# Performance work log

Hardware: AMD Instinct MI355X
Metric: run time of the kernel (lower is better)

The kernel has to match this reference:

```python
import jax, jax.numpy as jnp
import numpy as np

E = 4096      # hidden_size
H = 32        # num_attention_heads
D = E // H    # head_dim = 128
PAST = 8191   # past kv length


def setup_inputs() -> dict:
    key = jax.random.key(0)
    ks = jax.random.split(key, 10)
    s = 0.02
    return {
        "hidden_states": jax.random.normal(ks[0], (1, 1, E), jnp.float32),
        "past_key": jax.random.normal(ks[1], (1, D, PAST), jnp.float32),
        "past_value": jax.random.normal(ks[2], (1, PAST, D), jnp.float32),
        "attention_mask": jnp.zeros((1, 1, 1, PAST + 1), jnp.float32),
        "q_w": jax.random.normal(ks[3], (E, E), jnp.float32) * s,
        "q_b": jnp.zeros((E,), jnp.float32),
        "kv_w": jax.random.normal(ks[4], (E, 2 * D), jnp.float32) * s,
        "kv_b": jnp.zeros((2 * D,), jnp.float32),
        "proj_w": jax.random.normal(ks[5], (E, E), jnp.float32) * s,
        "proj_b": jnp.zeros((E,), jnp.float32),
    }


def reference(hidden_states, past_key, past_value, attention_mask,
              q_w, q_b, kv_w, kv_b, proj_w, proj_b):
    B, S = hidden_states.shape[:2]  # B=1, S=1 (decode)
    # Conv1D projections: x @ W + b
    query = hidden_states @ q_w + q_b            # [B, S, E]
    kv = hidden_states @ kv_w + kv_b             # [B, S, 2D]
    key_new, value_new = kv[..., :D], kv[..., D:]  # [B, S, D] each

    q = query.reshape(B, S, H, D).transpose(0, 2, 1, 3)  # [B, H, S, D]
    key_perm = key_new.transpose(0, 2, 1)                 # [B, D, S]
    full_key = jnp.concatenate([past_key, key_perm], axis=-1)     # [B, D, K]
    full_value = jnp.concatenate([past_value, value_new], axis=-2)  # [B, K, D]
    K = full_key.shape[-1]

    # QK^T with shared single KV head, scaled by sqrt(head_dim)
    scores = jnp.einsum('bhqd,bdk->bhqk', q, full_key)  # [B, H, S, K]
    scores = scores / jnp.asarray(D ** 0.5, scores.dtype)

    # causal mask over rows [K-S, K)
    causal = (jnp.arange(K)[None, :] <= (jnp.arange(S) + (K - S))[:, None])  # [S, K]
    mask_value = jnp.asarray(jnp.finfo(scores.dtype).min, scores.dtype)
    scores = jnp.where(causal[None, None], scores, mask_value)
    scores = scores + attention_mask

    attn_weights = jax.nn.softmax(scores, axis=-1)                # [B, H, S, K]
    attn_out = jnp.einsum('bhqk,bkd->bhqd', attn_weights, full_value)  # [B, H, S, D]
    attn_out = attn_out.transpose(0, 2, 1, 3).reshape(B, S, E)    # merge heads
    attn_out = attn_out @ proj_w + proj_b                          # [B, S, E]
    return attn_out, key_perm, value_new
```

## Files before the change

kernel.cpp:

```cpp
#include <hip/hip_runtime.h>
#include <math.h>

#define E_DIM 4096
#define H_NUM 32
#define D_DIM 128
#define PAST_K 8191
#define K_TOT 8192

typedef float f32x4 __attribute__((ext_vector_type(4)));

#define WS_QUERY 0
#define WS_KV    4096
#define WS_PQ    4608
#define WS_PA    (WS_PQ + 256*4352)
#define WS_PL    (WS_PA + 128*4096)
#define WS_PP    (WS_PL + 4096)

__global__ void __launch_bounds__(576, 2)
k_qkv(const float* __restrict__ hs,
      const float* __restrict__ q_w,
      const float* __restrict__ kv_w,
      float* __restrict__ ws) {
    const int t = threadIdx.x;
    const int e0 = blockIdx.y * 16;
    if (t < 512) {
        const int o = blockIdx.x * 2048 + t * 4;
        float ax = 0.f, ay = 0.f, az = 0.f, aw = 0.f;
#pragma unroll
        for (int i = 0; i < 16; ++i) {
            const int e = e0 + i;
            const float x = hs[e];
            const float4 w = *reinterpret_cast<const float4*>(q_w + (size_t)e * E_DIM + o);
            ax += x * w.x; ay += x * w.y; az += x * w.z; aw += x * w.w;
        }
        *reinterpret_cast<float4*>(ws + WS_PQ + (size_t)blockIdx.y * 4352 + o) =
            make_float4(ax, ay, az, aw);
    } else if (blockIdx.x == 0) {
        const int o = (t - 512) * 4;
        float ax = 0.f, ay = 0.f, az = 0.f, aw = 0.f;
#pragma unroll
        for (int i = 0; i < 16; ++i) {
            const int e = e0 + i;
            const float x = hs[e];
            const float4 w = *reinterpret_cast<const float4*>(kv_w + (size_t)e * 256 + o);
            ax += x * w.x; ay += x * w.y; az += x * w.z; aw += x * w.w;
        }
        *reinterpret_cast<float4*>(ws + WS_PQ + (size_t)blockIdx.y * 4352 + 4096 + o) =
            make_float4(ax, ay, az, aw);
    }
}

__global__ void __launch_bounds__(256, 4)
k_qkv_reduce(const float* __restrict__ q_b, const float* __restrict__ kv_b,
             float* __restrict__ ws, float* __restrict__ out) {
    __shared__ f32x4 rr[32][8];
    const int t = threadIdx.x;
    const int ol = t & 7;
    const int sg = t >> 3;
    const int o = blockIdx.x * 32 + ol * 4;
    f32x4 acc = {0.f, 0.f, 0.f, 0.f};
#pragma unroll
    for (int s = sg * 8; s < sg * 8 + 8; ++s)
        acc += *reinterpret_cast<const f32x4*>(ws + WS_PQ + (size_t)s * 4352 + o);
    rr[sg][ol] = acc;
    __syncthreads();
    if (t < 8) {
        f32x4 v = {0.f, 0.f, 0.f, 0.f};
#pragma unroll
        for (int g = 0; g < 32; ++g) v += rr[g][t];
        const int oo = blockIdx.x * 32 + t * 4;
        if (oo < 4096) {
#pragma unroll
            for (int j = 0; j < 4; ++j) ws[WS_QUERY + oo + j] = v[j] + q_b[oo + j];
        } else {
            const int i = oo - 4096;
#pragma unroll
            for (int j = 0; j < 4; ++j) {
                const float r = v[j] + kv_b[i + j];
                ws[WS_KV + i + j] = r;
                out[oo + j] = r;
            }
        }
    }
}

__global__ void __launch_bounds__(512, 2)
k_attn(const float* __restrict__ past_key,
       const float* __restrict__ past_value,
       const float* __restrict__ mask,
       float* __restrict__ ws) {
    __shared__ float sq[8 * 128];
    __shared__ float sp[8 * 64];
    __shared__ float red[4096];
    const int t = threadIdx.x;
    const int hy = blockIdx.y;
    const int kx = blockIdx.x;
    const int h0 = hy * 8;
    const int k0 = kx * 64;
    const float* __restrict__ kvn = ws + WS_KV;

    sq[t]       = ws[WS_QUERY + h0 * D_DIM + t];
    sq[t + 512] = ws[WS_QUERY + h0 * D_DIM + t + 512];
    __syncthreads();

    const int kl = t & 63;
    const int team = t >> 6;
    const int d0 = team * 16;
    const int k = k0 + kl;
    const bool tailA = (k == PAST_K);
    const float* kp = tailA ? (kvn + d0) : (past_key + (size_t)d0 * PAST_K + k);
    const size_t kstr = tailA ? 1 : PAST_K;

    float acc[8];
#pragma unroll
    for (int h = 0; h < 8; ++h) acc[h] = 0.f;

#pragma unroll
    for (int i = 0; i < 16; i += 4) {
        const float v0 = kp[0];
        const float v1 = kp[kstr];
        const float v2 = kp[2 * kstr];
        const float v3 = kp[3 * kstr];
        kp += 4 * kstr;
#pragma unroll
        for (int h = 0; h < 8; ++h) {
            const float4 q = *reinterpret_cast<const float4*>(&sq[h * 128 + d0 + i]);
            acc[h] += q.x * v0 + q.y * v1 + q.z * v2 + q.w * v3;
        }
    }
#pragma unroll
    for (int h = 0; h < 8; ++h)
        red[(team * 8 + h) * 64 + kl] = acc[h];
    __syncthreads();

    {
        const float scale = 0.08838834764831845f;
        const float mk = mask[k];
        float s = 0.f;
#pragma unroll
        for (int tp = 0; tp < 8; ++tp) s += red[(tp * 8 + team) * 64 + kl];
        const float e = __expf(s * scale + mk);
        sp[team * 64 + kl] = e;
        float l = e;
#pragma unroll
        for (int off = 32; off > 0; off >>= 1) l += __shfl_xor(l, off);
        if (kl == 0)
            ws[WS_PL + ((size_t)(kx * 4 + hy)) * 8 + team] = l;
    }
    __syncthreads();

    const int d = t & 127;
    const int kg = t >> 7;
    const int kb = k0 + kg * 16;
    const float* __restrict__ vp = past_value + (size_t)kb * D_DIM + d;
    const float* __restrict__ vlast =
        (kb + 15 == PAST_K) ? (kvn + D_DIM + d) : (vp + 15 * (size_t)D_DIM);

    float b[8];
#pragma unroll
    for (int h = 0; h < 8; ++h) b[h] = 0.f;

#pragma unroll
    for (int kk = 0; kk < 15; ++kk) {
        const float v = vp[(size_t)kk * D_DIM];
#pragma unroll
        for (int h = 0; h < 8; ++h) b[h] += sp[h * 64 + kg * 16 + kk] * v;
    }
    {
        const float v = *vlast;
#pragma unroll
        for (int h = 0; h < 8; ++h) b[h] += sp[h * 64 + kg * 16 + 15] * v;
    }
#pragma unroll
    for (int h = 0; h < 8; ++h)
        red[(kg * 8 + h) * 128 + d] = b[h];
    __syncthreads();

#pragma unroll
    for (int j = 0; j < 2; ++j) {
        const int hh = kg * 2 + j;
        const float s = red[(0 * 8 + hh) * 128 + d] + red[(1 * 8 + hh) * 128 + d] +
                        red[(2 * 8 + hh) * 128 + d] + red[(3 * 8 + hh) * 128 + d];
        ws[WS_PA + (size_t)kx * 4096 + (h0 + hh) * D_DIM + d] = s;
    }
}

__global__ void __launch_bounds__(512, 2)
k_proj(const float* __restrict__ proj_w,
       float* __restrict__ ws) {
    __shared__ float sred[32 * 16];
    __shared__ float lpart[2];
    __shared__ float sa[16];
    const int t = threadIdx.x;
    const int by = blockIdx.y;
    const int e0 = by * 16;
    const int h  = by >> 3;

    {
        const int el = t & 15;
        const int kg = t >> 4;
        float ps = 0.f;
#pragma unroll
        for (int j = 0; j < 4; ++j)
            ps += ws[WS_PA + (size_t)(kg * 4 + j) * 4096 + e0 + el];
        sred[kg * 16 + el] = ps;
    }
    if (t < 128) {
        float lv = ws[WS_PL + (size_t)t * 32 + (h >> 3) * 8 + (h & 7)];
#pragma unroll
        for (int off = 32; off > 0; off >>= 1) lv += __shfl_xor(lv, off);
        if ((t & 63) == 0) lpart[t >> 6] = lv;
    }
    __syncthreads();
    if (t < 16) {
        float asum = 0.f;
#pragma unroll
        for (int g = 0; g < 32; ++g) asum += sred[g * 16 + t];
        sa[t] = asum / (lpart[0] + lpart[1]);
    }
    __syncthreads();

    const int o = blockIdx.x * 2048 + t * 4;
    float ax = 0.f, ay = 0.f, az = 0.f, aw = 0.f;
#pragma unroll
    for (int i = 0; i < 16; ++i) {
        const float x = sa[i];
        const float4 w = *reinterpret_cast<const float4*>(proj_w + (size_t)(e0 + i) * E_DIM + o);
        ax += x * w.x; ay += x * w.y; az += x * w.z; aw += x * w.w;
    }
    *reinterpret_cast<float4*>(ws + WS_PP + (size_t)by * 4096 + o) =
        make_float4(ax, ay, az, aw);
}

__global__ void __launch_bounds__(256, 4)
k_proj_reduce(const float* __restrict__ proj_b,
              float* __restrict__ ws, float* __restrict__ out) {
    __shared__ f32x4 rr[32][8];
    const int t = threadIdx.x;
    const int ol = t & 7;
    const int sg = t >> 3;
    const int o = blockIdx.x * 32 + ol * 4;
    f32x4 acc = {0.f, 0.f, 0.f, 0.f};
#pragma unroll
    for (int s = sg * 8; s < sg * 8 + 8; ++s)
        acc += *reinterpret_cast<const f32x4*>(ws + WS_PP + (size_t)s * 4096 + o);
    rr[sg][ol] = acc;
    __syncthreads();
    if (t < 8) {
        f32x4 v = {0.f, 0.f, 0.f, 0.f};
#pragma unroll
        for (int g = 0; g < 32; ++g) v += rr[g][t];
        const int oo = blockIdx.x * 32 + t * 4;
        const f32x4 bb = *reinterpret_cast<const f32x4*>(proj_b + oo);
        *reinterpret_cast<f32x4*>(out + oo) = v + bb;
    }
}

extern "C" void kernel_launch(void* const* d_in, const int* in_sizes, int n_in,
                              void* d_out, int out_size, void* d_ws, size_t ws_size,
                              hipStream_t stream) {
    const float* hs      = (const float*)d_in[0];
    const float* past_k  = (const float*)d_in[1];
    const float* past_v  = (const float*)d_in[2];
    const float* mask    = (const float*)d_in[3];
    const float* q_w     = (const float*)d_in[4];
    const float* q_b     = (const float*)d_in[5];
    const float* kv_w    = (const float*)d_in[6];
    const float* kv_b    = (const float*)d_in[7];
    const float* proj_w  = (const float*)d_in[8];
    const float* proj_b  = (const float*)d_in[9];
    float* out = (float*)d_out;
    float* ws  = (float*)d_ws;

    k_qkv        <<<dim3(2, 256), dim3(576), 0, stream>>>(hs, q_w, kv_w, ws);
    k_qkv_reduce <<<dim3(136),    dim3(256), 0, stream>>>(q_b, kv_b, ws, out);
    k_attn       <<<dim3(128, 4), dim3(512), 0, stream>>>(past_k, past_v, mask, ws);
    k_proj       <<<dim3(2, 256), dim3(512), 0, stream>>>(proj_w, ws);
    k_proj_reduce<<<dim3(128),    dim3(256), 0, stream>>>(proj_b, ws, out);
}
```

Before: 187.3 us.

## Fuse split-K GEMV and reduction kernels via inter-block flag synchronization

Merges the QKV GEMV with its reduction kernel, and the output projection GEMV with its reduction kernel, into single launches. Producer blocks publish partial sums with agent-scope atomic stores and set per-block flags; reducer blocks in the same grid spin on those flags. The flags are reset inside the attention kernel for the next call. Each producer block now handles 32 input rows instead of 16. This cuts launches from five to three and removes the tail gaps between them, at the cost of spin-waiting and relying on all blocks being co-resident to avoid deadlock.

```diff
diff --git a/kernel.cpp b/kernel.cpp
--- a/kernel.cpp
+++ b/kernel.cpp
@@ -12,73 +12,142 @@
 #define WS_QUERY 0
 #define WS_KV    4096
 #define WS_PQ    4608
-#define WS_PA    (WS_PQ + 256*4352)
+#define WS_PKV   (WS_PQ + 128*4096)
+#define WS_PA    (WS_PKV + 16*256)
 #define WS_PL    (WS_PA + 128*4096)
 #define WS_PP    (WS_PL + 4096)
-
-__global__ void __launch_bounds__(576, 2)
-k_qkv(const float* __restrict__ hs,
-      const float* __restrict__ q_w,
-      const float* __restrict__ kv_w,
-      float* __restrict__ ws) {
+#define WS_FLAGS (WS_PP + 128*4096)
+
+#define MAGIC  0x3A91C27D
+#define NFLAG1 272
+#define NFLAG3 256
+
+__device__ inline void st_agent_f2(float* p, float a, float b) {
+    union { float f[2]; unsigned long long u; } v;
+    v.f[0] = a; v.f[1] = b;
+    __hip_atomic_store(reinterpret_cast<unsigned long long*>(p), v.u,
+                       __ATOMIC_RELAXED, __HIP_MEMORY_SCOPE_AGENT);
+}
+
+__device__ inline void set_flag(int* f) {
+    asm volatile("" ::: "memory");
+    __hip_atomic_store(f, MAGIC, __ATOMIC_RELAXED, __HIP_MEMORY_SCOPE_AGENT);
+}
+
+__device__ inline void spin_flag(const int* f) {
+    while (__hip_atomic_load(f, __ATOMIC_RELAXED, __HIP_MEMORY_SCOPE_AGENT) != MAGIC)
+        __builtin_amdgcn_s_sleep(8);
+}
+
+__global__ void __launch_bounds__(512, 2)
+k_qkv_f(const float* __restrict__ hs,
+        const float* __restrict__ q_w,
+        const float* __restrict__ kv_w,
+        const float* __restrict__ q_b,
+        const float* __restrict__ kv_b,
+        float* __restrict__ ws, float* __restrict__ out) {
+    __shared__ f32x4 sm[576];
+    int* flags = reinterpret_cast<int*>(ws + WS_FLAGS);
+    const int id = blockIdx.x;
     const int t = threadIdx.x;
-    const int e0 = blockIdx.y * 16;
-    if (t < 512) {
-        const int o = blockIdx.x * 2048 + t * 4;
+
+    if (id < 256) {
+        const int strip = id >> 7;
+        const int by = id & 127;
+        const int e0 = by * 32;
+        const int o = strip * 2048 + t * 4;
         float ax = 0.f, ay = 0.f, az = 0.f, aw = 0.f;
 #pragma unroll
-        for (int i = 0; i < 16; ++i) {
-            const int e = e0 + i;
-            const float x = hs[e];
-            const float4 w = *reinterpret_cast<const float4*>(q_w + (size_t)e * E_DIM + o);
+        for (int i = 0; i < 32; ++i) {
+            const float x = hs[e0 + i];
+            const float4 w = *reinterpret_cast<const float4*>(q_w + (size_t)(e0 + i) * E_DIM + o);
             ax += x * w.x; ay += x * w.y; az += x * w.z; aw += x * w.w;
         }
-        *reinterpret_cast<float4*>(ws + WS_PQ + (size_t)blockIdx.y * 4352 + o) =
-            make_float4(ax, ay, az, aw);
-    } else if (blockIdx.x == 0) {
-        const int o = (t - 512) * 4;
+        float* p = ws + WS_PQ + (size_t)by * 4096 + o;
+        st_agent_f2(p, ax, ay);
+        st_agent_f2(p + 2, az, aw);
+        __syncthreads();
+        if (t == 0) set_flag(&flags[id]);
+    } else if (id < 272) {
+        const int k = id - 256;
+        const int ol = t & 63;
+        const int rg = t >> 6;
+        const int o = ol * 4;
         float ax = 0.f, ay = 0.f, az = 0.f, aw = 0.f;
 #pragma unroll
-        for (int i = 0; i < 16; ++i) {
-            const int e = e0 + i;
-            const float x = hs[e];
-            const float4 w = *reinterpret_cast<const float4*>(kv_w + (size_t)e * 256 + o);
+        for (int i = 0; i < 32; ++i) {
+            const int r = k * 256 + rg * 32 + i;
+            const float x = hs[r];
+            const float4 w = *reinterpret_cast<const float4*>(kv_w + (size_t)r * 256 + o);
             ax += x * w.x; ay += x * w.y; az += x * w.z; aw += x * w.w;
         }
-        *reinterpret_cast<float4*>(ws + WS_PQ + (size_t)blockIdx.y * 4352 + 4096 + o) =
-            make_float4(ax, ay, az, aw);
-    }
-}
-
-__global__ void __launch_bounds__(256, 4)
-k_qkv_reduce(const float* __restrict__ q_b, const float* __restrict__ kv_b,
-             float* __restrict__ ws, float* __restrict__ out) {
-    __shared__ f32x4 rr[32][8];
-    const int t = threadIdx.x;
-    const int ol = t & 7;
-    const int sg = t >> 3;
-    const int o = blockIdx.x * 32 + ol * 4;
-    f32x4 acc = {0.f, 0.f, 0.f, 0.f};
-#pragma unroll
-    for (int s = sg * 8; s < sg * 8 + 8; ++s)
-        acc += *reinterpret_cast<const f32x4*>(ws + WS_PQ + (size_t)s * 4352 + o);
-    rr[sg][ol] = acc;
-    __syncthreads();
-    if (t < 8) {
-        f32x4 v = {0.f, 0.f, 0.f, 0.f};
-#pragma unroll
-        for (int g = 0; g < 32; ++g) v += rr[g][t];
-        const int oo = blockIdx.x * 32 + t * 4;
-        if (oo < 4096) {
-#pragma unroll
-            for (int j = 0; j < 4; ++j) ws[WS_QUERY + oo + j] = v[j] + q_b[oo + j];
+        sm[rg * 64 + ol] = (f32x4){ax, ay, az, aw};
+        __syncthreads();
+        if (t < 64) {
+            f32x4 v = {0.f, 0.f, 0.f, 0.f};
+#pragma unroll
+            for (int g = 0; g < 8; ++g) v += sm[g * 64 + t];
+            float* p = ws + WS_PKV + k * 256 + t * 4;
+            st_agent_f2(p, v.x, v.y);
+            st_agent_f2(p + 2, v.z, v.w);
+        }
+        __syncthreads();
+        if (t == 0) set_flag(&flags[256 + k]);
+    } else {
+        const int c = id - 272;
+        if (c < 128) {
+            const int o0 = c * 32;
+            const int s = c >> 6;
+            if (t < 128) spin_flag(&flags[s * 128 + t]);
+            __syncthreads();
+            if (t == 0) (void)__hip_atomic_load(&flags[s * 128], __ATOMIC_ACQUIRE,
+                                                __HIP_MEMORY_SCOPE_AGENT);
+            __syncthreads();
+            const int ol = t & 7, sg = t >> 3;
+            const int o = o0 + ol * 4;
+            f32x4 acc = *reinterpret_cast<const f32x4*>(ws + WS_PQ + (size_t)(2 * sg) * 4096 + o)
+                      + *reinterpret_cast<const f32x4*>(ws + WS_PQ + (size_t)(2 * sg + 1) * 4096 + o);
+            sm[sg * 8 + ol] = acc;
+            __syncthreads();
+            if (t < 64) {
+                const int sup = t >> 3, l = t & 7;
+                f32x4 v = {0.f, 0.f, 0.f, 0.f};
+#pragma unroll
+                for (int j = 0; j < 8; ++j) v += sm[(sup * 8 + j) * 8 + l];
+                sm[512 + sup * 8 + l] = v;
+            }
+            __syncthreads();
+            if (t < 8) {
+                f32x4 v = {0.f, 0.f, 0.f, 0.f};
+#pragma unroll
+                for (int s2 = 0; s2 < 8; ++s2) v += sm[512 + s2 * 8 + t];
+                const int oo = o0 + t * 4;
+#pragma unroll
+                for (int j = 0; j < 4; ++j) ws[WS_QUERY + oo + j] = v[j] + q_b[oo + j];
+            }
         } else {
-            const int i = oo - 4096;
-#pragma unroll
-            for (int j = 0; j < 4; ++j) {
-                const float r = v[j] + kv_b[i + j];
-                ws[WS_KV + i + j] = r;
-                out[oo + j] = r;
+            const int o0k = (c - 128) * 32;
+            if (t < 16) spin_flag(&flags[256 + t]);
+            __syncthreads();
+            if (t == 0) (void)__hip_atomic_load(&flags[256], __ATOMIC_ACQUIRE,
+                                                __HIP_MEMORY_SCOPE_AGENT);
+            __syncthreads();
+            if (t < 128) {
+                const int ol = t & 7, sg = t >> 3;
+                sm[sg * 8 + ol] = *reinterpret_cast<const f32x4*>(ws + WS_PKV + sg * 256 + o0k + ol * 4);
+            }
+            __syncthreads();
+            if (t < 8) {
+                f32x4 v = {0.f, 0.f, 0.f, 0.f};
+#pragma unroll
+                for (int g = 0; g < 16; ++g) v += sm[g * 8 + t];
+                const int i0 = o0k + t * 4;
+#pragma unroll
+                for (int j = 0; j < 4; ++j) {
+                    const float r = v[j] + kv_b[i0 + j];
+                    ws[WS_KV + i0 + j] = r;
+                    out[4096 + i0 + j] = r;
+                }
             }
         }
     }
@@ -99,6 +168,12 @@
     const int k0 = kx * 64;
     const float* __restrict__ kvn = ws + WS_KV;
 
+    if (kx == 0 && hy == 0) {
+        int* flags = reinterpret_cast<int*>(ws + WS_FLAGS);
+        flags[t] = 0;
+        if (t < 16) flags[512 + t] = 0;
+    }
+
     sq[t]       = ws[WS_QUERY + h0 * D_DIM + t];
     sq[t + 512] = ws[WS_QUERY + h0 * D_DIM + t + 512];
     __syncthreads();
@@ -186,73 +261,89 @@
 }
 
 __global__ void __launch_bounds__(512, 2)
-k_proj(const float* __restrict__ proj_w,
-       float* __restrict__ ws) {
-    __shared__ float sred[32 * 16];
+k_proj_f(const float* __restrict__ proj_w,
+         const float* __restrict__ proj_b,
+         float* __restrict__ ws, float* __restrict__ out) {
+    __shared__ f32x4 sm[576];
+    __shared__ float sred[16 * 32];
     __shared__ float lpart[2];
-    __shared__ float sa[16];
+    __shared__ float sa[32];
+    int* flags = reinterpret_cast<int*>(ws + WS_FLAGS);
+    const int id = blockIdx.x;
     const int t = threadIdx.x;
-    const int by = blockIdx.y;
-    const int e0 = by * 16;
-    const int h  = by >> 3;
-
-    {
-        const int el = t & 15;
-        const int kg = t >> 4;
-        float ps = 0.f;
-#pragma unroll
-        for (int j = 0; j < 4; ++j)
-            ps += ws[WS_PA + (size_t)(kg * 4 + j) * 4096 + e0 + el];
-        sred[kg * 16 + el] = ps;
-    }
-    if (t < 128) {
-        float lv = ws[WS_PL + (size_t)t * 32 + (h >> 3) * 8 + (h & 7)];
-#pragma unroll
-        for (int off = 32; off > 0; off >>= 1) lv += __shfl_xor(lv, off);
-        if ((t & 63) == 0) lpart[t >> 6] = lv;
-    }
-    __syncthreads();
-    if (t < 16) {
-        float asum = 0.f;
-#pragma unroll
-        for (int g = 0; g < 32; ++g) asum += sred[g * 16 + t];
-        sa[t] = asum / (lpart[0] + lpart[1]);
-    }
-    __syncthreads();
-
-    const int o = blockIdx.x * 2048 + t * 4;
-    float ax = 0.f, ay = 0.f, az = 0.f, aw = 0.f;
-#pragma unroll
-    for (int i = 0; i < 16; ++i) {
-        const float x = sa[i];
-        const float4 w = *reinterpret_cast<const float4*>(proj_w + (size_t)(e0 + i) * E_DIM + o);
-        ax += x * w.x; ay += x * w.y; az += x * w.z; aw += x * w.w;
-    }
-    *reinterpret_cast<float4*>(ws + WS_PP + (size_t)by * 4096 + o) =
-        make_float4(ax, ay, az, aw);
-}
-
-__global__ void __launch_bounds__(256, 4)
-k_proj_reduce(const float* __restrict__ proj_b,
-              float* __restrict__ ws, float* __restrict__ out) {
-    __shared__ f32x4 rr[32][8];
-    const int t = threadIdx.x;
-    const int ol = t & 7;
-    const int sg = t >> 3;
-    const int o = blockIdx.x * 32 + ol * 4;
-    f32x4 acc = {0.f, 0.f, 0.f, 0.f};
-#pragma unroll
-    for (int s = sg * 8; s < sg * 8 + 8; ++s)
-        acc += *reinterpret_cast<const f32x4*>(ws + WS_PP + (size_t)s * 4096 + o);
-    rr[sg][ol] = acc;
-    __syncthreads();
-    if (t < 8) {
-        f32x4 v = {0.f, 0.f, 0.f, 0.f};
-#pragma unroll
-        for (int g = 0; g < 32; ++g) v += rr[g][t];
-        const int oo = blockIdx.x * 32 + t * 4;
-        const f32x4 bb = *reinterpret_cast<const f32x4*>(proj_b + oo);
-        *reinterpret_cast<f32x4*>(out + oo) = v + bb;
+
+    if (id < 256) {
+        const int strip = id >> 7;
+        const int by = id & 127;
+        const int e0 = by * 32;
+        const int h = by >> 2;
+        {
+            const int el = t & 31, kg = t >> 5;
+            float ps = 0.f;
+#pragma unroll
+            for (int j = 0; j < 8; ++j)
+                ps += ws[WS_PA + (size_t)(kg * 8 + j) * 4096 + e0 + el];
+            sred[kg * 32 + el] = ps;
+        }
+        if (t < 128) {
+            float lv = ws[WS_PL + (size_t)t * 32 + (h >> 3) * 8 + (h & 7)];
+#pragma unroll
+            for (int off = 32; off > 0; off >>= 1) lv += __shfl_xor(lv, off);
+            if ((t & 63) == 0) lpart[t >> 6] = lv;
+        }
+        __syncthreads();
+        if (t < 32) {
+            float asum = 0.f;
+#pragma unroll
+            for (int g = 0; g < 16; ++g) asum += sred[g * 32 + t];
+            sa[t] = asum / (lpart[0] + lpart[1]);
+        }
+        __syncthreads();
+
+        const int o = strip * 2048 + t * 4;
+        float ax = 0.f, ay = 0.f, az = 0.f, aw = 0.f;
+#pragma unroll
+        for (int i = 0; i < 32; ++i) {
+            const float x = sa[i];
+            const float4 w = *reinterpret_cast<const float4*>(proj_w + (size_t)(e0 + i) * E_DIM + o);
+            ax += x * w.x; ay += x * w.y; az += x * w.z; aw += x * w.w;
+        }
+        float* p = ws + WS_PP + (size_t)by * 4096 + o;
+        st_agent_f2(p, ax, ay);
+        st_agent_f2(p + 2, az, aw);
+        __syncthreads();
+        if (t == 0) set_flag(&flags[NFLAG1 + id]);
+    } else {
+        const int c = id - 256;
+        const int o0 = c * 32;
+        const int s = c >> 6;
+        if (t < 128) spin_flag(&flags[NFLAG1 + s * 128 + t]);
+        __syncthreads();
+        if (t == 0) (void)__hip_atomic_load(&flags[NFLAG1 + s * 128], __ATOMIC_ACQUIRE,
+                                            __HIP_MEMORY_SCOPE_AGENT);
+        __syncthreads();
+        const int ol = t & 7, sg = t >> 3;
+        const int o = o0 + ol * 4;
+        f32x4 acc = *reinterpret_cast<const f32x4*>(ws + WS_PP + (size_t)(2 * sg) * 4096 + o)
+                  + *reinterpret_cast<const f32x4*>(ws + WS_PP + (size_t)(2 * sg + 1) * 4096 + o);
+        sm[sg * 8 + ol] = acc;
+        __syncthreads();
+        if (t < 64) {
+            const int sup = t >> 3, l = t & 7;
+            f32x4 v = {0.f, 0.f, 0.f, 0.f};
+#pragma unroll
+            for (int j = 0; j < 8; ++j) v += sm[(sup * 8 + j) * 8 + l];
+            sm[512 + sup * 8 + l] = v;
+        }
+        __syncthreads();
+        if (t < 8) {
+            f32x4 v = {0.f, 0.f, 0.f, 0.f};
+#pragma unroll
+            for (int s2 = 0; s2 < 8; ++s2) v += sm[512 + s2 * 8 + t];
+            const int oo = o0 + t * 4;
+            const f32x4 bb = *reinterpret_cast<const f32x4*>(proj_b + oo);
+            *reinterpret_cast<f32x4*>(out + oo) = v + bb;
+        }
     }
 }
 
@@ -272,9 +363,7 @@
     float* out = (float*)d_out;
     float* ws  = (float*)d_ws;
 
-    k_qkv        <<<dim3(2, 256), dim3(576), 0, stream>>>(hs, q_w, kv_w, ws);
-    k_qkv_reduce <<<dim3(136),    dim3(256), 0, stream>>>(q_b, kv_b, ws, out);
-    k_attn       <<<dim3(128, 4), dim3(512), 0, stream>>>(past_k, past_v, mask, ws);
-    k_proj       <<<dim3(2, 256), dim3(512), 0, stream>>>(proj_w, ws);
-    k_proj_reduce<<<dim3(128),    dim3(256), 0, stream>>>(proj_b, ws, out);
-}
+    k_qkv_f <<<dim3(408),    dim3(512), 0, stream>>>(hs, q_w, kv_w, q_b, kv_b, ws, out);
+    k_attn  <<<dim3(128, 4), dim3(512), 0, stream>>>(past_k, past_v, mask, ws);
+    k_proj_f<<<dim3(384),    dim3(512), 0, stream>>>(proj_w, proj_b, ws, out);
+}
```

Result: slower. 194.9 us (+4.1%).
